# Performance work log

Hardware: AMD Instinct MI355X
Metric: run time of the kernel (lower is better)

## Reference

```python
import jax, jax.numpy as jnp
import numpy as np

B, N, D_IN, D_OUT, L, T = 8, 512, 1024, 1024, 16, 4096


def setup_inputs() -> dict:
    key = jax.random.key(0)
    k1, k2, k3 = jax.random.split(key, 3)
    pooled_vectors = jax.random.normal(k1, (B, N, D_IN), dtype=jnp.float32)
    # stacked nn.Linear weights, each (out, in), bias=False
    W = jax.random.normal(k2, (L, D_OUT, D_IN), dtype=jnp.float32) * 0.02
    pooling_indices = jnp.sort(jax.random.randint(k3, (N,), 0, T, dtype=jnp.int64))
    return {
        "pooled_vectors": pooled_vectors,
        "W": W,
        "pooling_indices": pooling_indices,
        "target_length": T,
    }


def reference(pooled_vectors, W, pooling_indices, target_length):
    # pooled_vectors: (B, N, D_in); W: (L, D_out, D_in); pooling_indices: (N,) sorted
    Bn, Nn, _ = pooled_vectors.shape
    Ln = W.shape[0]
    t = jnp.arange(target_length)
    # segment i covers [start_i, idx_i + 1); searchsorted finds the covering segment
    seg = jnp.searchsorted(pooling_indices, t, side="left")  # (T,)
    valid = seg < Nn  # positions past the last pooling index stay zero
    segc = jnp.clip(seg, 0, Nn - 1)
    start = jnp.where(segc > 0, pooling_indices[segc - 1] + 1, 0)
    lidx = jnp.minimum(t - start, Ln - 1)  # position-specific linear index, capped
    # apply all L position linears to every pooled vector: (B, N, L, D_out)
    trans = jnp.einsum("bnd,lod->bnlo", pooled_vectors, W)
    out = trans[:, segc, lidx]  # gather per output position -> (B, T, D_out)
    return jnp.where(valid[None, :, None], out, jnp.zeros((), out.dtype))
```

## Files before the change

kernel.cpp:

```cpp
#include <hip/hip_runtime.h>
#include <stdint.h>

#define B_    8
#define N_    512
#define DIN   1024
#define DOUT  1024
#define L_    16
#define T_    4096

#define BM 128
#define BN 128
#define BK 64
#define NB (DOUT / BN)
#define MT_MAX 272
#define ZROW ((long)B_ * N_)

typedef __attribute__((ext_vector_type(8))) short short8;
typedef __attribute__((ext_vector_type(4))) float f32x4;

#define POOLED_ELEMS ((long)B_ * N_ * DIN + DIN)
#define WS_W_OFF     ((size_t)POOLED_ELEMS * 2)
#define WS_META_OFF  (WS_W_OFF + (size_t)L_ * DOUT * DIN * 2)

__device__ __forceinline__ unsigned short f2bf(float f) {
  unsigned u = __float_as_uint(f);
  u += 0x7FFFu + ((u >> 16) & 1u);
  return (unsigned short)(u >> 16);
}

__device__ __forceinline__ void gload_lds16(const void* g, void* l) {
  __builtin_amdgcn_global_load_lds(
      (const __attribute__((address_space(1))) void*)g,
      (__attribute__((address_space(3))) void*)l, 16, 0, 0);
}

__global__ void k_convert(const float* __restrict__ pooled,
                          const float* __restrict__ W,
                          unsigned short* __restrict__ wsP,
                          unsigned short* __restrict__ wsW) {
  const long np4 = (long)B_ * N_ * DIN / 4;
  const long nw4 = (long)L_ * DOUT * DIN / 4;
  const long nz4 = DIN / 4;
  long i = (long)blockIdx.x * blockDim.x + threadIdx.x;
  const long stride = (long)gridDim.x * blockDim.x;
  for (; i < np4 + nw4 + nz4; i += stride) {
    if (i < np4) {
      float4 v = ((const float4*)pooled)[i];
      ushort4 o = { f2bf(v.x), f2bf(v.y), f2bf(v.z), f2bf(v.w) };
      ((ushort4*)wsP)[i] = o;
    } else if (i < np4 + nw4) {
      float4 v = ((const float4*)W)[i - np4];
      ushort4 o = { f2bf(v.x), f2bf(v.y), f2bf(v.z), f2bf(v.w) };
      ((ushort4*)wsW)[i - np4] = o;
    } else {
      ushort4 z = {0, 0, 0, 0};
      ((ushort4*)wsP)[i - nw4] = z;
    }
  }
}

__global__ void k_map(const int* __restrict__ pidx, int* __restrict__ map) {
  int t = blockIdx.x * blockDim.x + threadIdx.x;
  if (t >= T_) return;
  int lo = 0, hi = N_;
  while (lo < hi) {
    int mid = (lo + hi) >> 1;
    if (pidx[mid] < t) lo = mid + 1; else hi = mid;
  }
  int n, lidx;
  if (lo < N_) {
    int start = (lo > 0) ? (pidx[lo - 1] + 1) : 0;
    int li = t - start;
    lidx = li > (L_ - 1) ? (L_ - 1) : li;
    n = lo;
  } else {
    n = 0xFFFF;
    lidx = L_ - 1;
  }
  map[t] = n | (lidx << 16);
}

__global__ void k_group(const int* __restrict__ map,
                        unsigned* __restrict__ tlist,
                        int* __restrict__ goff, int* __restrict__ grows,
                        unsigned* __restrict__ table, int* __restrict__ ntiles) {
  __shared__ int cnt[L_];
  __shared__ int pos[L_];
  int tid = threadIdx.x;
  if (tid < L_) cnt[tid] = 0;
  __syncthreads();
  for (int t = tid; t < T_; t += 256)
    atomicAdd(&cnt[(map[t] >> 16) & 0xFFFF], 1);
  __syncthreads();
  if (tid == 0) {
    int off = 0;
    for (int l = 0; l < L_; ++l) {
      pos[l] = off; goff[l] = off; grows[l] = cnt[l] * B_;
      off += cnt[l];
    }
  }
  __syncthreads();
  for (int t = tid; t < T_; t += 256) {
    int m = map[t];
    int l = (m >> 16) & 0xFFFF;
    int p = atomicAdd(&pos[l], 1);
    tlist[p] = (unsigned)t | ((unsigned)(m & 0xFFFF) << 16);
  }
  __syncthreads();
  if (tid == 0) {
    int tt = 0;
    for (int l = 0; l < L_; ++l) {
      int rows = cnt[l] * B_;
      for (int r0 = 0; r0 < rows; r0 += BM)
        table[tt++] = (unsigned)l | ((unsigned)r0 << 4);
    }
    *ntiles = tt;
  }
}

__global__ void k_gemm(const unsigned short* __restrict__ wsP,
                       const unsigned short* __restrict__ wsW,
                       const unsigned* __restrict__ tlist,
                       const int* __restrict__ goff,
                       const int* __restrict__ grows,
                       const unsigned* __restrict__ table,
                       const int* __restrict__ ntiles,
                       float* __restrict__ out) {
  const int bid = blockIdx.x;
  const int mt = bid / NB;
  const int nt = bid % NB;
  if (mt >= *ntiles) return;

  const unsigned te = table[mt];
  const int l    = te & 15;
  const int row0 = (int)(te >> 4);
  const int toff = goff[l];
  const int rows = grows[l];

  __shared__ __align__(16) unsigned short As[BM * BK];
  __shared__ __align__(16) unsigned short Bs[BM * BK];

  const int tid  = threadIdx.x;
  const int w    = tid >> 6;
  const int lane = tid & 63;
  const int inoff = (lane & 7) * 16;

  const unsigned short* arow[4];
  const unsigned short* brow[4];
  const unsigned short* wbase = wsW + (long)l * DOUT * DIN + (long)nt * BN * DIN;
#pragma unroll
  for (int i = 0; i < 4; ++i) {
    int r  = i * 32 + w * 8 + (lane >> 3);
    int rg = row0 + r;
    long rowElem;
    if (rg < rows) {
      unsigned e = tlist[toff + (rg >> 3)];
      unsigned n = e >> 16;
      int b = rg & 7;
      rowElem = (n == 0xFFFFu) ? ZROW * DIN : ((long)(b * N_ + (int)n)) * DIN;
    } else {
      rowElem = ZROW * DIN;
    }
    arow[i] = wsP + rowElem;
    brow[i] = wbase + (long)r * DIN;
  }

  f32x4 acc[4][4];
#pragma unroll
  for (int m = 0; m < 4; ++m)
#pragma unroll
    for (int n = 0; n < 4; ++n)
      acc[m][n] = (f32x4){0.f, 0.f, 0.f, 0.f};

  const int wmRow = (w >> 1) * 64;
  const int wnCol = (w & 1) * 64;

  for (int ks = 0; ks < DIN / BK; ++ks) {
    const int k0b = ks * BK * 2;
    __syncthreads();
#pragma unroll
    for (int i = 0; i < 4; ++i)
      gload_lds16((const char*)arow[i] + k0b + inoff,
                  (char*)As + (i * 32 + w * 8) * (BK * 2));
#pragma unroll
    for (int i = 0; i < 4; ++i)
      gload_lds16((const char*)brow[i] + k0b + inoff,
                  (char*)Bs + (i * 32 + w * 8) * (BK * 2));
    __syncthreads();

#pragma unroll
    for (int ks2 = 0; ks2 < 2; ++ks2) {
      short8 af[4], bf[4];
      const int kb = ks2 * 32 + (lane >> 4) * 8;
#pragma unroll
      for (int m = 0; m < 4; ++m)
        af[m] = *(const short8*)(As + (wmRow + m * 16 + (lane & 15)) * BK + kb);
#pragma unroll
      for (int n = 0; n < 4; ++n)
        bf[n] = *(const short8*)(Bs + (wnCol + n * 16 + (lane & 15)) * BK + kb);
#pragma unroll
      for (int m = 0; m < 4; ++m)
#pragma unroll
        for (int n = 0; n < 4; ++n)
          acc[m][n] = __builtin_amdgcn_mfma_f32_16x16x32_bf16(
              af[m], bf[n], acc[m][n], 0, 0, 0);
    }
  }

#pragma unroll
  for (int m = 0; m < 4; ++m) {
#pragma unroll
    for (int j = 0; j < 4; ++j) {
      int rt = wmRow + m * 16 + (lane >> 4) * 4 + j;
      int rg = row0 + rt;
      if (rg >= rows) continue;
      unsigned e = tlist[toff + (rg >> 3)];
      int b = rg & 7;
      int t = (int)(e & 0xFFFFu);
      float* orow = out + ((long)b * T_ + t) * DOUT + nt * BN + wnCol + (lane & 15);
#pragma unroll
      for (int n = 0; n < 4; ++n)
        orow[n * 16] = acc[m][n][j];
    }
  }
}

extern "C" void kernel_launch(void* const* d_in, const int* in_sizes, int n_in,
                              void* d_out, int out_size, void* d_ws, size_t ws_size,
                              hipStream_t stream) {
  const float* pooled = (const float*)d_in[0];
  const float* W      = (const float*)d_in[1];
  const int*   pidx   = (const int*)d_in[2];
  float* out = (float*)d_out;

  char* ws = (char*)d_ws;
  unsigned short* wsP = (unsigned short*)(ws);
  unsigned short* wsW = (unsigned short*)(ws + WS_W_OFF);
  int* meta  = (int*)(ws + WS_META_OFF);
  int* map   = meta;
  unsigned* tlist = (unsigned*)(meta + T_);
  int* goff  = meta + 2 * T_;
  int* grows = meta + 2 * T_ + 16;
  unsigned* table = (unsigned*)(meta + 2 * T_ + 32);
  int* ntiles = meta + 2 * T_ + 32 + MT_MAX;

  k_convert<<<2048, 256, 0, stream>>>(pooled, W, wsP, wsW);
  k_map<<<(T_ + 255) / 256, 256, 0, stream>>>(pidx, map);
  k_group<<<1, 256, 0, stream>>>(map, tlist, goff, grows, table, ntiles);
  k_gemm<<<MT_MAX * NB, 256, 0, stream>>>(wsP, wsW, tlist, goff, grows, table,
                                          ntiles, out);
}
```

Before: 138.9 us.

## Triple-buffer GEMM K loop with swizzled LDS and 256-row tiles

Rewrites the grouped GEMM so each block handles 256 rows with 512 threads (8 waves, each owning a 64x64 output sub-tile). Global-to-LDS loads go into a three-stage ring buffer with explicit vmcnt waits, so loads for tile k+2 overlap the MFMA work on tile k. An XOR swizzle on the LDS layout is meant to avoid bank conflicts, and s_setprio is raised around the MFMA bursts. The aim is to hide memory latency and reuse the W tile across more rows. The cost is more LDS, fewer tiles at launch, and more padded waste in the last tile of each length group.

```diff
diff --git a/kernel.cpp b/kernel.cpp
--- a/kernel.cpp
+++ b/kernel.cpp
@@ -8,11 +8,12 @@
 #define L_    16
 #define T_    4096
 
-#define BM 128
+#define BM 256
 #define BN 128
 #define BK 64
 #define NB (DOUT / BN)
-#define MT_MAX 272
+#define NKT (DIN / BK)
+#define MT_MAX 144
 #define ZROW ((long)B_ * N_)
 
 typedef __attribute__((ext_vector_type(8))) short short8;
@@ -32,6 +33,12 @@
   __builtin_amdgcn_global_load_lds(
       (const __attribute__((address_space(1))) void*)g,
       (__attribute__((address_space(3))) void*)l, 16, 0, 0);
+}
+
+__device__ __forceinline__ void bar() {
+  asm volatile("" ::: "memory");
+  __builtin_amdgcn_s_barrier();
+  asm volatile("" ::: "memory");
 }
 
 __global__ void k_convert(const float* __restrict__ pooled,
@@ -118,17 +125,18 @@
   }
 }
 
-__global__ void k_gemm(const unsigned short* __restrict__ wsP,
-                       const unsigned short* __restrict__ wsW,
-                       const unsigned* __restrict__ tlist,
-                       const int* __restrict__ goff,
-                       const int* __restrict__ grows,
-                       const unsigned* __restrict__ table,
-                       const int* __restrict__ ntiles,
-                       float* __restrict__ out) {
+__global__ __launch_bounds__(512, 1)
+void k_gemm(const unsigned short* __restrict__ wsP,
+            const unsigned short* __restrict__ wsW,
+            const unsigned* __restrict__ tlist,
+            const int* __restrict__ goff,
+            const int* __restrict__ grows,
+            const unsigned* __restrict__ table,
+            const int* __restrict__ ntiles,
+            float* __restrict__ out) {
   const int bid = blockIdx.x;
-  const int mt = bid / NB;
-  const int nt = bid % NB;
+  const int mt = bid >> 3;
+  const int nt = bid & 7;
   if (mt >= *ntiles) return;
 
   const unsigned te = table[mt];
@@ -137,33 +145,48 @@
   const int toff = goff[l];
   const int rows = grows[l];
 
-  __shared__ __align__(16) unsigned short As[BM * BK];
-  __shared__ __align__(16) unsigned short Bs[BM * BK];
+  __shared__ __align__(16) unsigned short As[3][BM * BK];
+  __shared__ __align__(16) unsigned short Bs[3][BN * BK];
 
   const int tid  = threadIdx.x;
+  const int lane = tid & 63;
   const int w    = tid >> 6;
-  const int lane = tid & 63;
-  const int inoff = (lane & 7) * 16;
-
-  const unsigned short* arow[4];
-  const unsigned short* brow[4];
-  const unsigned short* wbase = wsW + (long)l * DOUT * DIN + (long)nt * BN * DIN;
+  const int wm   = w >> 1;
+  const int wn   = w & 1;
+
+  const int srow = tid >> 3;
+  const int sxor = ((tid & 7) ^ (srow & 7)) * 16;
+  const char* aptr[4];
 #pragma unroll
   for (int i = 0; i < 4; ++i) {
-    int r  = i * 32 + w * 8 + (lane >> 3);
-    int rg = row0 + r;
+    int rg = row0 + i * 64 + srow;
     long rowElem;
     if (rg < rows) {
       unsigned e = tlist[toff + (rg >> 3)];
       unsigned n = e >> 16;
       int b = rg & 7;
-      rowElem = (n == 0xFFFFu) ? ZROW * DIN : ((long)(b * N_ + (int)n)) * DIN;
+      rowElem = (n == 0xFFFFu) ? ZROW * (long)DIN
+                               : ((long)(b * N_ + (int)n)) * DIN;
     } else {
-      rowElem = ZROW * DIN;
-    }
-    arow[i] = wsP + rowElem;
-    brow[i] = wbase + (long)r * DIN;
-  }
+      rowElem = ZROW * (long)DIN;
+    }
+    aptr[i] = (const char*)(wsP + rowElem) + sxor;
+  }
+  const char* bptr[2];
+#pragma unroll
+  for (int i = 0; i < 2; ++i)
+    bptr[i] = (const char*)(wsW +
+              ((long)l * DOUT + nt * BN + i * 64 + srow) * DIN) + sxor;
+
+#define STAGE_A(i, kt, nb) \
+  gload_lds16(aptr[i] + (kt) * 128, (char*)As[nb] + (i) * 8192 + w * 1024)
+#define STAGE_B(i, kt, nb) \
+  gload_lds16(bptr[i] + (kt) * 128, (char*)Bs[nb] + (i) * 8192 + w * 1024)
+
+  const int arb = (wm * 64 + (lane & 15)) * BK;
+  const int brb = (wn * 64 + (lane & 15)) * BK;
+  const int ax0 = (((lane >> 4) + 0) ^ (lane & 7)) * 8;
+  const int ax1 = (((lane >> 4) + 4) ^ (lane & 7)) * 8;
 
   f32x4 acc[4][4];
 #pragma unroll
@@ -172,57 +195,86 @@
     for (int n = 0; n < 4; ++n)
       acc[m][n] = (f32x4){0.f, 0.f, 0.f, 0.f};
 
-  const int wmRow = (w >> 1) * 64;
-  const int wnCol = (w & 1) * 64;
-
-  for (int ks = 0; ks < DIN / BK; ++ks) {
-    const int k0b = ks * BK * 2;
-    __syncthreads();
-#pragma unroll
-    for (int i = 0; i < 4; ++i)
-      gload_lds16((const char*)arow[i] + k0b + inoff,
-                  (char*)As + (i * 32 + w * 8) * (BK * 2));
-#pragma unroll
-    for (int i = 0; i < 4; ++i)
-      gload_lds16((const char*)brow[i] + k0b + inoff,
-                  (char*)Bs + (i * 32 + w * 8) * (BK * 2));
-    __syncthreads();
-
-#pragma unroll
-    for (int ks2 = 0; ks2 < 2; ++ks2) {
-      short8 af[4], bf[4];
-      const int kb = ks2 * 32 + (lane >> 4) * 8;
-#pragma unroll
-      for (int m = 0; m < 4; ++m)
-        af[m] = *(const short8*)(As + (wmRow + m * 16 + (lane & 15)) * BK + kb);
-#pragma unroll
-      for (int n = 0; n < 4; ++n)
-        bf[n] = *(const short8*)(Bs + (wnCol + n * 16 + (lane & 15)) * BK + kb);
-#pragma unroll
-      for (int m = 0; m < 4; ++m)
-#pragma unroll
-        for (int n = 0; n < 4; ++n)
-          acc[m][n] = __builtin_amdgcn_mfma_f32_16x16x32_bf16(
-              af[m], bf[n], acc[m][n], 0, 0, 0);
-    }
+  STAGE_A(0, 0, 0); STAGE_A(1, 0, 0); STAGE_A(2, 0, 0);
+  STAGE_A(3, 0, 0); STAGE_B(0, 0, 0); STAGE_B(1, 0, 0);
+  STAGE_A(0, 1, 1); STAGE_A(1, 1, 1); STAGE_A(2, 1, 1);
+  STAGE_A(3, 1, 1); STAGE_B(0, 1, 1); STAGE_B(1, 1, 1);
+  asm volatile("s_waitcnt vmcnt(6)" ::: "memory");
+  bar();
+
+  int buf = 0;
+  for (int t = 0; t < NKT; ++t) {
+    const unsigned short* Ab = As[buf];
+    const unsigned short* Bb = Bs[buf];
+    const int nb = (buf >= 1) ? buf - 1 : buf + 2;
+    const int kt2 = t + 2;
+
+    short8 af[4][2], bf[4][2];
+
+#pragma unroll
+    for (int m = 0; m < 4; ++m) {
+      af[m][0] = *(const short8*)(Ab + arb + m * 1024 + ax0);
+      af[m][1] = *(const short8*)(Ab + arb + m * 1024 + ax1);
+    }
+#pragma unroll
+    for (int n = 0; n < 2; ++n) {
+      bf[n][0] = *(const short8*)(Bb + brb + n * 1024 + ax0);
+      bf[n][1] = *(const short8*)(Bb + brb + n * 1024 + ax1);
+    }
+    if (kt2 < NKT) { STAGE_A(0, kt2, nb); STAGE_A(1, kt2, nb); STAGE_A(2, kt2, nb); }
+    bar();
+    __builtin_amdgcn_s_setprio(1);
+#pragma unroll
+    for (int n = 0; n < 2; ++n)
+#pragma unroll
+      for (int m = 0; m < 4; ++m) {
+        acc[m][n] = __builtin_amdgcn_mfma_f32_16x16x32_bf16(af[m][0], bf[n][0], acc[m][n], 0, 0, 0);
+        acc[m][n] = __builtin_amdgcn_mfma_f32_16x16x32_bf16(af[m][1], bf[n][1], acc[m][n], 0, 0, 0);
+      }
+    __builtin_amdgcn_s_setprio(0);
+    bar();
+
+#pragma unroll
+    for (int n = 2; n < 4; ++n) {
+      bf[n][0] = *(const short8*)(Bb + brb + n * 1024 + ax0);
+      bf[n][1] = *(const short8*)(Bb + brb + n * 1024 + ax1);
+    }
+    if (kt2 < NKT) { STAGE_A(3, kt2, nb); STAGE_B(0, kt2, nb); STAGE_B(1, kt2, nb); }
+    bar();
+    __builtin_amdgcn_s_setprio(1);
+#pragma unroll
+    for (int n = 2; n < 4; ++n)
+#pragma unroll
+      for (int m = 0; m < 4; ++m) {
+        acc[m][n] = __builtin_amdgcn_mfma_f32_16x16x32_bf16(af[m][0], bf[n][0], acc[m][n], 0, 0, 0);
+        acc[m][n] = __builtin_amdgcn_mfma_f32_16x16x32_bf16(af[m][1], bf[n][1], acc[m][n], 0, 0, 0);
+      }
+    __builtin_amdgcn_s_setprio(0);
+    if (t <= NKT - 3)      asm volatile("s_waitcnt vmcnt(6)" ::: "memory");
+    else if (t == NKT - 2) asm volatile("s_waitcnt vmcnt(0)" ::: "memory");
+    bar();
+
+    buf = (buf == 2) ? 0 : buf + 1;
   }
 
 #pragma unroll
   for (int m = 0; m < 4; ++m) {
 #pragma unroll
     for (int j = 0; j < 4; ++j) {
-      int rt = wmRow + m * 16 + (lane >> 4) * 4 + j;
+      int rt = wm * 64 + m * 16 + (lane >> 4) * 4 + j;
       int rg = row0 + rt;
       if (rg >= rows) continue;
       unsigned e = tlist[toff + (rg >> 3)];
       int b = rg & 7;
-      int t = (int)(e & 0xFFFFu);
-      float* orow = out + ((long)b * T_ + t) * DOUT + nt * BN + wnCol + (lane & 15);
+      int tt = (int)(e & 0xFFFFu);
+      float* orow = out + ((long)b * T_ + tt) * DOUT + nt * BN + wn * 64 + (lane & 15);
 #pragma unroll
       for (int n = 0; n < 4; ++n)
         orow[n * 16] = acc[m][n][j];
     }
   }
+#undef STAGE_A
+#undef STAGE_B
 }
 
 extern "C" void kernel_launch(void* const* d_in, const int* in_sizes, int n_in,
@@ -247,6 +299,6 @@
   k_convert<<<2048, 256, 0, stream>>>(pooled, W, wsP, wsW);
   k_map<<<(T_ + 255) / 256, 256, 0, stream>>>(pidx, map);
   k_group<<<1, 256, 0, stream>>>(map, tlist, goff, grows, table, ntiles);
-  k_gemm<<<MT_MAX * NB, 256, 0, stream>>>(wsP, wsW, tlist, goff, grows, table,
+  k_gemm<<<MT_MAX * NB, 512, 0, stream>>>(wsP, wsW, tlist, goff, grows, table,
                                           ntiles, out);
 }
```

Result: slower. 148.8 us (+7.1%).

## Use 256x256 double-buffered GEMM tiles with swizzled LDS and fused prep kernel

Applied to the files above, without the earlier changes.

Grows the GEMM tile to 256x256 with 512 threads and double-buffered LDS. Global-to-LDS loads for the next K tile are interleaved with MFMA quads, using explicit waitcnt, barriers and setprio. LDS rows are XOR-swizzled to avoid bank conflicts, and the map and group preprocessing kernels are merged into one kernel that works in shared memory. The larger tiles reuse more data per load, but padding waste grows for small per-L groups and the pipeline adds register pressure and more barriers.

```diff
diff --git a/kernel.cpp b/kernel.cpp
--- a/kernel.cpp
+++ b/kernel.cpp
@@ -8,11 +8,13 @@
 #define L_    16
 #define T_    4096
 
-#define BM 128
-#define BN 128
+#define BM 256
+#define BN 256
 #define BK 64
 #define NB (DOUT / BN)
-#define MT_MAX 272
+#define NKT (DIN / BK)
+#define NIT (NKT / 2)
+#define MT_MAX 160
 #define ZROW ((long)B_ * N_)
 
 typedef __attribute__((ext_vector_type(8))) short short8;
@@ -32,6 +34,12 @@
   __builtin_amdgcn_global_load_lds(
       (const __attribute__((address_space(1))) void*)g,
       (__attribute__((address_space(3))) void*)l, 16, 0, 0);
+}
+
+__device__ __forceinline__ void bar() {
+  asm volatile("" ::: "memory");
+  __builtin_amdgcn_s_barrier();
+  asm volatile("" ::: "memory");
 }
 
 __global__ void k_convert(const float* __restrict__ pooled,
@@ -59,38 +67,30 @@
   }
 }
 
-__global__ void k_map(const int* __restrict__ pidx, int* __restrict__ map) {
-  int t = blockIdx.x * blockDim.x + threadIdx.x;
-  if (t >= T_) return;
-  int lo = 0, hi = N_;
-  while (lo < hi) {
-    int mid = (lo + hi) >> 1;
-    if (pidx[mid] < t) lo = mid + 1; else hi = mid;
-  }
-  int n, lidx;
-  if (lo < N_) {
-    int start = (lo > 0) ? (pidx[lo - 1] + 1) : 0;
-    int li = t - start;
-    lidx = li > (L_ - 1) ? (L_ - 1) : li;
-    n = lo;
-  } else {
-    n = 0xFFFF;
-    lidx = L_ - 1;
-  }
-  map[t] = n | (lidx << 16);
-}
-
-__global__ void k_group(const int* __restrict__ map,
-                        unsigned* __restrict__ tlist,
-                        int* __restrict__ goff, int* __restrict__ grows,
-                        unsigned* __restrict__ table, int* __restrict__ ntiles) {
-  __shared__ int cnt[L_];
-  __shared__ int pos[L_];
-  int tid = threadIdx.x;
+__global__ void k_prep(const int* __restrict__ pidx,
+                       unsigned* __restrict__ tlist,
+                       int* __restrict__ goff, int* __restrict__ grows,
+                       unsigned* __restrict__ table, int* __restrict__ ntiles) {
+  __shared__ int sp[N_];
+  __shared__ unsigned smap[T_];
+  __shared__ int cnt[L_], pos[L_];
+  const int tid = threadIdx.x;
+  for (int i = tid; i < N_; i += 256) sp[i] = pidx[i];
   if (tid < L_) cnt[tid] = 0;
   __syncthreads();
-  for (int t = tid; t < T_; t += 256)
-    atomicAdd(&cnt[(map[t] >> 16) & 0xFFFF], 1);
+  for (int t = tid; t < T_; t += 256) {
+    int lo = 0, hi = N_;
+    while (lo < hi) { int mid = (lo + hi) >> 1; if (sp[mid] < t) lo = mid + 1; else hi = mid; }
+    int n, l;
+    if (lo < N_) {
+      int start = lo ? sp[lo - 1] + 1 : 0;
+      int li = t - start;
+      l = li > (L_ - 1) ? (L_ - 1) : li;
+      n = lo;
+    } else { n = 0xFFFF; l = L_ - 1; }
+    smap[t] = (unsigned)n | ((unsigned)l << 16);
+    atomicAdd(&cnt[l], 1);
+  }
   __syncthreads();
   if (tid == 0) {
     int off = 0;
@@ -101,34 +101,34 @@
   }
   __syncthreads();
   for (int t = tid; t < T_; t += 256) {
-    int m = map[t];
-    int l = (m >> 16) & 0xFFFF;
+    unsigned m = smap[t];
+    int l = m >> 16;
     int p = atomicAdd(&pos[l], 1);
-    tlist[p] = (unsigned)t | ((unsigned)(m & 0xFFFF) << 16);
+    tlist[p] = (unsigned)t | ((m & 0xFFFFu) << 16);
   }
   __syncthreads();
   if (tid == 0) {
     int tt = 0;
     for (int l = 0; l < L_; ++l) {
       int rows = cnt[l] * B_;
-      for (int r0 = 0; r0 < rows; r0 += BM)
-        table[tt++] = (unsigned)l | ((unsigned)r0 << 4);
+      for (int r0 = 0; r0 < rows; r0 += BM) table[tt++] = (unsigned)l | ((unsigned)r0 << 4);
     }
     *ntiles = tt;
   }
 }
 
-__global__ void k_gemm(const unsigned short* __restrict__ wsP,
-                       const unsigned short* __restrict__ wsW,
-                       const unsigned* __restrict__ tlist,
-                       const int* __restrict__ goff,
-                       const int* __restrict__ grows,
-                       const unsigned* __restrict__ table,
-                       const int* __restrict__ ntiles,
-                       float* __restrict__ out) {
+__global__ __launch_bounds__(512, 2)
+void k_gemm(const unsigned short* __restrict__ wsP,
+            const unsigned short* __restrict__ wsW,
+            const unsigned* __restrict__ tlist,
+            const int* __restrict__ goff,
+            const int* __restrict__ grows,
+            const unsigned* __restrict__ table,
+            const int* __restrict__ ntiles,
+            float* __restrict__ out) {
   const int bid = blockIdx.x;
-  const int mt = bid / NB;
-  const int nt = bid % NB;
+  const int mt = bid >> 2;
+  const int nt = bid & 3;
   if (mt >= *ntiles) return;
 
   const unsigned te = table[mt];
@@ -137,92 +137,143 @@
   const int toff = goff[l];
   const int rows = grows[l];
 
-  __shared__ __align__(16) unsigned short As[BM * BK];
-  __shared__ __align__(16) unsigned short Bs[BM * BK];
+  __shared__ __align__(16) unsigned short As[2][BM * BK];
+  __shared__ __align__(16) unsigned short Bs[2][BN * BK];
 
   const int tid  = threadIdx.x;
+  const int lane = tid & 63;
   const int w    = tid >> 6;
-  const int lane = tid & 63;
-  const int inoff = (lane & 7) * 16;
-
-  const unsigned short* arow[4];
-  const unsigned short* brow[4];
-  const unsigned short* wbase = wsW + (long)l * DOUT * DIN + (long)nt * BN * DIN;
-#pragma unroll
-  for (int i = 0; i < 4; ++i) {
-    int r  = i * 32 + w * 8 + (lane >> 3);
-    int rg = row0 + r;
-    long rowElem;
-    if (rg < rows) {
-      unsigned e = tlist[toff + (rg >> 3)];
-      unsigned n = e >> 16;
-      int b = rg & 7;
-      rowElem = (n == 0xFFFFu) ? ZROW * DIN : ((long)(b * N_ + (int)n)) * DIN;
-    } else {
-      rowElem = ZROW * DIN;
-    }
-    arow[i] = wsP + rowElem;
-    brow[i] = wbase + (long)r * DIN;
-  }
-
-  f32x4 acc[4][4];
-#pragma unroll
-  for (int m = 0; m < 4; ++m)
+  const int wm   = w >> 2;
+  const int wn   = w & 3;
+
+  const int srow = tid >> 3;
+  const int sxor = ((tid & 7) ^ (srow & 7)) * 16;
+  const char* aptr[4];
+  const char* bptr[4];
+#pragma unroll
+  for (int h = 0; h < 2; ++h)
+#pragma unroll
+    for (int r = 0; r < 2; ++r) {
+      int rt = h * 128 + r * 64 + srow;
+      int rg = row0 + rt;
+      long rowElem;
+      if (rg < rows) {
+        unsigned e = tlist[toff + (rg >> 3)];
+        unsigned n = e >> 16;
+        int b = rg & 7;
+        rowElem = (n == 0xFFFFu) ? ZROW * (long)DIN
+                                 : ((long)(b * N_ + (int)n)) * DIN;
+      } else rowElem = ZROW * (long)DIN;
+      aptr[h * 2 + r] = (const char*)(wsP + rowElem) + sxor;
+      bptr[h * 2 + r] = (const char*)(wsW + ((long)l * DOUT + nt * BN + rt) * DIN) + sxor;
+    }
+
+#define STG_A(h, kt, bb) do { \
+  gload_lds16(aptr[(h)*2+0] + (kt)*128, (char*)As[bb] + (((h)*128 + w*8)*128)); \
+  gload_lds16(aptr[(h)*2+1] + (kt)*128, (char*)As[bb] + (((h)*128 + 64 + w*8)*128)); } while (0)
+#define STG_B(h, kt, bb) do { \
+  gload_lds16(bptr[(h)*2+0] + (kt)*128, (char*)Bs[bb] + (((h)*128 + w*8)*128)); \
+  gload_lds16(bptr[(h)*2+1] + (kt)*128, (char*)Bs[bb] + (((h)*128 + 64 + w*8)*128)); } while (0)
+
+  const int aoff = (wm * 128 + (lane & 15)) * 128;
+  const int boff = (wn * 64  + (lane & 15)) * 128;
+  const int ax0  = (((lane >> 4)    ) ^ (lane & 7)) * 16;
+  const int ax1  = (((lane >> 4) + 4) ^ (lane & 7)) * 16;
+
+#define DS_AF(bb, mo) do { _Pragma("unroll") \
+  for (int m_ = 0; m_ < 4; ++m_) { \
+    af[m_][0] = *(const short8*)((const char*)As[bb] + aoff + ((mo)+m_)*2048 + ax0); \
+    af[m_][1] = *(const short8*)((const char*)As[bb] + aoff + ((mo)+m_)*2048 + ax1); } } while (0)
+#define DS_BF(bb, no) do { _Pragma("unroll") \
+  for (int n_ = 0; n_ < 2; ++n_) { \
+    bf[(no)+n_][0] = *(const short8*)((const char*)Bs[bb] + boff + ((no)+n_)*2048 + ax0); \
+    bf[(no)+n_][1] = *(const short8*)((const char*)Bs[bb] + boff + ((no)+n_)*2048 + ax1); } } while (0)
+#define QUAD(mo, no) do { _Pragma("unroll") \
+  for (int n_ = 0; n_ < 2; ++n_) { _Pragma("unroll") \
+    for (int m_ = 0; m_ < 4; ++m_) { \
+      acc[(mo)+m_][(no)+n_] = __builtin_amdgcn_mfma_f32_16x16x32_bf16(af[m_][0], bf[(no)+n_][0], acc[(mo)+m_][(no)+n_], 0, 0, 0); \
+      acc[(mo)+m_][(no)+n_] = __builtin_amdgcn_mfma_f32_16x16x32_bf16(af[m_][1], bf[(no)+n_][1], acc[(mo)+m_][(no)+n_], 0, 0, 0); } } } while (0)
+#define LGKM0 asm volatile("s_waitcnt lgkmcnt(0)" ::: "memory")
+#define P1 __builtin_amdgcn_s_setprio(1)
+#define P0 __builtin_amdgcn_s_setprio(0)
+
+  f32x4 acc[8][4];
+#pragma unroll
+  for (int m = 0; m < 8; ++m)
 #pragma unroll
     for (int n = 0; n < 4; ++n)
       acc[m][n] = (f32x4){0.f, 0.f, 0.f, 0.f};
 
-  const int wmRow = (w >> 1) * 64;
-  const int wnCol = (w & 1) * 64;
-
-  for (int ks = 0; ks < DIN / BK; ++ks) {
-    const int k0b = ks * BK * 2;
-    __syncthreads();
-#pragma unroll
-    for (int i = 0; i < 4; ++i)
-      gload_lds16((const char*)arow[i] + k0b + inoff,
-                  (char*)As + (i * 32 + w * 8) * (BK * 2));
-#pragma unroll
-    for (int i = 0; i < 4; ++i)
-      gload_lds16((const char*)brow[i] + k0b + inoff,
-                  (char*)Bs + (i * 32 + w * 8) * (BK * 2));
-    __syncthreads();
-
-#pragma unroll
-    for (int ks2 = 0; ks2 < 2; ++ks2) {
-      short8 af[4], bf[4];
-      const int kb = ks2 * 32 + (lane >> 4) * 8;
-#pragma unroll
-      for (int m = 0; m < 4; ++m)
-        af[m] = *(const short8*)(As + (wmRow + m * 16 + (lane & 15)) * BK + kb);
-#pragma unroll
-      for (int n = 0; n < 4; ++n)
-        bf[n] = *(const short8*)(Bs + (wnCol + n * 16 + (lane & 15)) * BK + kb);
-#pragma unroll
-      for (int m = 0; m < 4; ++m)
-#pragma unroll
-        for (int n = 0; n < 4; ++n)
-          acc[m][n] = __builtin_amdgcn_mfma_f32_16x16x32_bf16(
-              af[m], bf[n], acc[m][n], 0, 0, 0);
-    }
-  }
-
-#pragma unroll
-  for (int m = 0; m < 4; ++m) {
-#pragma unroll
-    for (int j = 0; j < 4; ++j) {
-      int rt = wmRow + m * 16 + (lane >> 4) * 4 + j;
+  short8 af[4][2], bf[4][2];
+
+  STG_A(0, 0, 0); STG_A(1, 0, 0); STG_B(0, 0, 0); STG_B(1, 0, 0);
+  STG_A(0, 1, 1);
+  asm volatile("s_waitcnt vmcnt(2)" ::: "memory");
+  bar();
+
+  for (int j = 0; j < NIT; ++j) {
+    const int t1 = 2 * j + 1, t2 = 2 * j + 2, t3 = 2 * j + 3;
+
+    DS_AF(0, 0); DS_BF(0, 0);
+    STG_A(1, t1, 1);
+    bar(); LGKM0; P1; QUAD(0, 0); P0; bar();
+
+    DS_BF(0, 2);
+    STG_B(0, t1, 1);
+    bar(); LGKM0; P1; QUAD(0, 2); P0; bar();
+
+    DS_AF(0, 4);
+    STG_B(1, t1, 1);
+    bar(); LGKM0; P1; QUAD(4, 0); P0; bar();
+
+    if (t2 < NKT) STG_A(0, t2, 0);
+    bar(); P1; QUAD(4, 2); P0;
+    if (j < NIT - 1) asm volatile("s_waitcnt vmcnt(2)" ::: "memory");
+    else             asm volatile("s_waitcnt vmcnt(0)" ::: "memory");
+    bar();
+
+    DS_AF(1, 0); DS_BF(1, 0);
+    if (t2 < NKT) STG_A(1, t2, 0);
+    bar(); LGKM0; P1; QUAD(0, 0); P0; bar();
+
+    DS_BF(1, 2);
+    if (t2 < NKT) STG_B(0, t2, 0);
+    bar(); LGKM0; P1; QUAD(0, 2); P0; bar();
+
+    DS_AF(1, 4);
+    if (t2 < NKT) STG_B(1, t2, 0);
+    bar(); LGKM0; P1; QUAD(4, 0); P0; bar();
+
+    if (t3 < NKT) STG_A(0, t3, 1);
+    bar(); P1; QUAD(4, 2); P0;
+    if (j < NIT - 1) asm volatile("s_waitcnt vmcnt(2)" ::: "memory");
+    bar();
+  }
+
+#pragma unroll
+  for (int m = 0; m < 8; ++m) {
+#pragma unroll
+    for (int jj = 0; jj < 4; ++jj) {
+      int rt = wm * 128 + m * 16 + (lane >> 4) * 4 + jj;
       int rg = row0 + rt;
       if (rg >= rows) continue;
       unsigned e = tlist[toff + (rg >> 3)];
       int b = rg & 7;
-      int t = (int)(e & 0xFFFFu);
-      float* orow = out + ((long)b * T_ + t) * DOUT + nt * BN + wnCol + (lane & 15);
+      int tt = (int)(e & 0xFFFFu);
+      float* orow = out + ((long)b * T_ + tt) * DOUT + nt * BN + wn * 64 + (lane & 15);
 #pragma unroll
       for (int n = 0; n < 4; ++n)
-        orow[n * 16] = acc[m][n][j];
-    }
-  }
+        orow[n * 16] = acc[m][n][jj];
+    }
+  }
+#undef STG_A
+#undef STG_B
+#undef DS_AF
+#undef DS_BF
+#undef QUAD
+#undef LGKM0
+#undef P1
+#undef P0
 }
 
 extern "C" void kernel_launch(void* const* d_in, const int* in_sizes, int n_in,
@@ -237,16 +288,14 @@
   unsigned short* wsP = (unsigned short*)(ws);
   unsigned short* wsW = (unsigned short*)(ws + WS_W_OFF);
   int* meta  = (int*)(ws + WS_META_OFF);
-  int* map   = meta;
-  unsigned* tlist = (unsigned*)(meta + T_);
-  int* goff  = meta + 2 * T_;
-  int* grows = meta + 2 * T_ + 16;
-  unsigned* table = (unsigned*)(meta + 2 * T_ + 32);
-  int* ntiles = meta + 2 * T_ + 32 + MT_MAX;
-
+  unsigned* tlist = (unsigned*)meta;
+  int* goff  = meta + T_;
+  int* grows = meta + T_ + 16;
+  unsigned* table = (unsigned*)(meta + T_ + 32);
+  int* ntiles = meta + T_ + 32 + MT_MAX;
+
+  k_prep<<<1, 256, 0, stream>>>(pidx, tlist, goff, grows, table, ntiles);
   k_convert<<<2048, 256, 0, stream>>>(pooled, W, wsP, wsW);
-  k_map<<<(T_ + 255) / 256, 256, 0, stream>>>(pidx, map);
-  k_group<<<1, 256, 0, stream>>>(map, tlist, goff, grows, table, ntiles);
-  k_gemm<<<MT_MAX * NB, 256, 0, stream>>>(wsP, wsW, tlist, goff, grows, table,
+  k_gemm<<<MT_MAX * NB, 512, 0, stream>>>(wsP, wsW, tlist, goff, grows, table,
                                           ntiles, out);
 }
```

After: 149.7 us. 7.8% more time.
